# Kernel tuning notes

Measured on AMD Instinct MI355X. Metric: run time of the kernel, lower is better.

## Reference

```python
import jax, jax.numpy as jnp
import numpy as np

N_SPK, N_UTT, D = 512, 64, 1024
EPS = 1e-6  # matches tf.math.l2_normalize default epsilon guard


def _l2norm(x, axis=-1):
    return x / jnp.sqrt(jnp.maximum(jnp.sum(x * x, axis=axis, keepdims=True), EPS))


def setup_inputs() -> dict:
    key = jax.random.key(0)
    k1, _ = jax.random.split(key)
    inputs = jax.random.normal(k1, (N_SPK, N_UTT, D), dtype=jnp.float32)
    w = jnp.asarray(10.0, dtype=jnp.float32)
    b = jnp.asarray(-5.0, dtype=jnp.float32)
    return {"inputs": inputs, "w": w, "b": b}


def reference(inputs, w, b):
    N, M, _ = inputs.shape
    # speaker centroids: mean over utterances -> [N, D]
    centroids = jnp.mean(inputs, axis=1)
    # utterance (exclusion) centroids: mean of the other M-1 utterances -> [N, M, D]
    ut_centroids = (jnp.sum(inputs, axis=1, keepdims=True) - inputs) / (M - 1)

    e = _l2norm(inputs)          # [N, M, D]
    c = _l2norm(centroids)       # [N, D]
    uc = _l2norm(ut_centroids)   # [N, M, D]

    # cosine sim of every utterance vs every speaker centroid -> [N, M, K]
    cos_all = jnp.einsum('nmd,kd->nmk', e, c)
    # same-speaker entries use the self-exclusion centroid
    cos_self = jnp.sum(e * uc, axis=-1)  # [N, M]
    eye = jnp.eye(N, dtype=inputs.dtype)[:, None, :]  # [N, 1, N]
    cos_sim = cos_all * (1.0 - eye) + cos_self[:, :, None] * eye

    sim = w * cos_sim + b  # [N, M, N]
    # softmax contrastive loss: -S_{j,i,j} + logsumexp_k S_{j,i,k}, summed
    lse = jax.nn.logsumexp(sim, axis=-1)            # [N, M]
    pos = jnp.einsum('nmn->nm', sim)                # diagonal along speaker axes
    loss = jnp.sum(lse - pos)
    return loss
```

## Files before the change

### kernel.cpp

```cpp
#include <hip/hip_runtime.h>
#include <stdint.h>

#define N_SPK 512
#define N_UTT 64
#define DIM   1024
#define NROWS (N_SPK * N_UTT)
#define EPS   1e-6f

#define BM 128
#define BN 128
#define BK 32
#define KTILES (DIM / BK)

typedef __attribute__((ext_vector_type(8))) short short8;
typedef __attribute__((ext_vector_type(4))) float f32x4;

__device__ __forceinline__ uint16_t f2bf(float f) {
    union { float f; uint32_t i; } un; un.f = f;
    uint32_t x = un.i;
    return (uint16_t)((x + 0x7fffu + ((x >> 16) & 1u)) >> 16);
}

__global__ __launch_bounds__(256) void prep_stream(
    const float* __restrict__ x, uint16_t* __restrict__ xb,
    float* __restrict__ Sg4, float* __restrict__ xxg)
{
    const int b    = blockIdx.x;
    const int n    = b >> 2;
    const int g    = b & 3;
    const int tid  = threadIdx.x;
    const int lane = tid & 63;
    const int w    = tid >> 6;

    const float* xn  = x  + (size_t)n * N_UTT * DIM;
    uint16_t*    xbn = xb + (size_t)n * N_UTT * DIM;
    const int m0 = g * 16 + w * 4;

    float4 v[16];
    #pragma unroll
    for (int i = 0; i < 4; ++i)
        #pragma unroll
        for (int j = 0; j < 4; ++j)
            v[i * 4 + j] = *(const float4*)(xn + (size_t)(m0 + i) * DIM + j * 256 + lane * 4);

    float Sp[16];
    #pragma unroll
    for (int j = 0; j < 16; ++j) Sp[j] = 0.f;
    float xx[4] = {0.f, 0.f, 0.f, 0.f};

    #pragma unroll
    for (int i = 0; i < 4; ++i) {
        #pragma unroll
        for (int j = 0; j < 4; ++j) {
            const float4 q = v[i * 4 + j];
            xx[i] += q.x * q.x + q.y * q.y + q.z * q.z + q.w * q.w;
            Sp[j * 4 + 0] += q.x; Sp[j * 4 + 1] += q.y;
            Sp[j * 4 + 2] += q.z; Sp[j * 4 + 3] += q.w;
            ushort4 o;
            o.x = f2bf(q.x); o.y = f2bf(q.y); o.z = f2bf(q.z); o.w = f2bf(q.w);
            *(ushort4*)(xbn + (size_t)(m0 + i) * DIM + j * 256 + lane * 4) = o;
        }
    }

    #pragma unroll
    for (int i = 0; i < 4; ++i) {
        float t = xx[i];
        #pragma unroll
        for (int off = 1; off < 64; off <<= 1) t += __shfl_xor(t, off);
        if (lane == 0) xxg[n * N_UTT + m0 + i] = t;
    }

    __shared__ float Sh[4][DIM];
    #pragma unroll
    for (int j = 0; j < 4; ++j)
        *(float4*)&Sh[w][j * 256 + lane * 4] =
            make_float4(Sp[j * 4], Sp[j * 4 + 1], Sp[j * 4 + 2], Sp[j * 4 + 3]);
    __syncthreads();

    const int d0 = tid * 4;
    float4 a = *(const float4*)&Sh[0][d0];
    const float4 b1 = *(const float4*)&Sh[1][d0];
    const float4 b2 = *(const float4*)&Sh[2][d0];
    const float4 b3 = *(const float4*)&Sh[3][d0];
    a.x += b1.x + b2.x + b3.x; a.y += b1.y + b2.y + b3.y;
    a.z += b1.z + b2.z + b3.z; a.w += b1.w + b2.w + b3.w;
    *(float4*)(Sg4 + ((size_t)g * N_SPK + n) * DIM + d0) = a;
}

__global__ __launch_bounds__(256) void centroid_kernel(
    const float* __restrict__ Sg4, uint16_t* __restrict__ cmat, float* __restrict__ ssqg)
{
    const int n   = blockIdx.x;
    const int tid = threadIdx.x;
    const int d0  = tid * 4;

    float4 S = *(const float4*)(Sg4 + ((size_t)0 * N_SPK + n) * DIM + d0);
    #pragma unroll
    for (int g = 1; g < 4; ++g) {
        const float4 p = *(const float4*)(Sg4 + ((size_t)g * N_SPK + n) * DIM + d0);
        S.x += p.x; S.y += p.y; S.z += p.z; S.w += p.w;
    }

    float css = S.x * S.x + S.y * S.y + S.z * S.z + S.w * S.w;
    #pragma unroll
    for (int off = 1; off < 64; off <<= 1) css += __shfl_xor(css, off);
    __shared__ float red[4];
    if ((tid & 63) == 0) red[tid >> 6] = css;
    __syncthreads();
    const float ssq = red[0] + red[1] + red[2] + red[3];

    const float scale = rsqrtf(fmaxf(ssq * (1.0f / 4096.f), EPS)) * (1.0f / 64.f);
    ushort4 o;
    o.x = f2bf(S.x * scale); o.y = f2bf(S.y * scale);
    o.z = f2bf(S.z * scale); o.w = f2bf(S.w * scale);
    *(ushort4*)(cmat + (size_t)n * DIM + d0) = o;
    if (tid == 0) ssqg[n] = ssq;
}

__global__ __launch_bounds__(256) void gemm_lse_kernel(
    const uint16_t* __restrict__ xb, const uint16_t* __restrict__ cmat,
    const float* __restrict__ xxg, const float* __restrict__ ssqg,
    const float* __restrict__ wp, const float* __restrict__ bp,
    float* __restrict__ sumexp4, float* __restrict__ pos)
{
    __shared__ uint16_t Asm[BM * BK];
    __shared__ uint16_t Bsm[BN * BK];
    __shared__ float    SeLDS[BM];

    const int tid   = threadIdx.x;
    const int lane  = tid & 63;
    const int wid   = tid >> 6;
    const int waveM = wid >> 1;
    const int waveN = wid & 1;

    const int bid = blockIdx.x;
    const int rt  = (bid & 7) | ((bid >> 5) << 3);
    const int ct  = (bid >> 3) & 3;

    const int rowBase = rt * BM;
    const int colBase = ct * BN;

    const uint16_t* gA[2];
    const uint16_t* gB[2];
    #pragma unroll
    for (int i = 0; i < 2; ++i) {
        const int s    = i * 256 + tid;
        const int srow = s >> 2;
        const int kc   = (s & 3) ^ ((srow >> 1) & 3);
        gA[i] = xb   + (size_t)(rowBase + srow) * DIM + kc * 8;
        gB[i] = cmat + (size_t)(colBase + srow) * DIM + kc * 8;
    }

    f32x4 acc[4][4];
    #pragma unroll
    for (int i = 0; i < 4; ++i)
        #pragma unroll
        for (int j = 0; j < 4; ++j)
            acc[i][j] = (f32x4){0.f, 0.f, 0.f, 0.f};

    const int cL  = lane & 15;
    const int q   = lane >> 4;
    const int key = (cL >> 1) & 3;
    const int kcs = q ^ key;

    for (int kt = 0; kt < KTILES; ++kt) {
        __syncthreads();
        const int ko = kt * BK;
        #pragma unroll
        for (int i = 0; i < 2; ++i) {
            __builtin_amdgcn_global_load_lds(
                (const __attribute__((address_space(1))) void*)(gA[i] + ko),
                (__attribute__((address_space(3))) void*)(&Asm[(i * 256 + wid * 64) * 8]),
                16, 0, 0);
            __builtin_amdgcn_global_load_lds(
                (const __attribute__((address_space(1))) void*)(gB[i] + ko),
                (__attribute__((address_space(3))) void*)(&Bsm[(i * 256 + wid * 64) * 8]),
                16, 0, 0);
        }
        __syncthreads();

        short8 a[4], b[4];
        #pragma unroll
        for (int bi = 0; bi < 4; ++bi)
            a[bi] = *(const short8*)&Asm[(waveM * 64 + bi * 16 + cL) * BK + kcs * 8];
        #pragma unroll
        for (int bj = 0; bj < 4; ++bj)
            b[bj] = *(const short8*)&Bsm[(waveN * 64 + bj * 16 + cL) * BK + kcs * 8];

        #pragma unroll
        for (int bi = 0; bi < 4; ++bi)
            #pragma unroll
            for (int bj = 0; bj < 4; ++bj)
                acc[bi][bj] = __builtin_amdgcn_mfma_f32_16x16x32_bf16(
                    a[bi], b[bj], acc[bi][bj], 0, 0, 0);
    }

    const float wv = wp[0], bv = bp[0];
    float srow[16];
    #pragma unroll
    for (int bi = 0; bi < 4; ++bi) {
        #pragma unroll
        for (int r = 0; r < 4; ++r) {
            const int R     = rowBase + waveM * 64 + bi * 16 + q * 4 + r;
            const float xxv = xxg[R];
            const float rn  = rsqrtf(fmaxf(xxv, EPS));
            const int nrow  = R >> 6;
            float s = 0.f;
            #pragma unroll
            for (int bj = 0; bj < 4; ++bj) {
                const int col = colBase + waveN * 64 + bj * 16 + cL;
                const float dot = acc[bi][bj][r];
                float sim;
                if (col == nrow) {
                    const float ssqv = ssqg[nrow];
                    const float xs   = dot * sqrtf(ssqv);
                    const float d2   = ssqv - 2.f * xs + xxv;
                    const float cs   = ((xs - xxv) * (1.f / 63.f)) * rn *
                                       rsqrtf(fmaxf(d2 * (1.f / 3969.f), EPS));
                    sim = wv * cs + bv;
                    pos[R] = sim;
                } else {
                    sim = wv * (dot * rn) + bv;
                }
                s += __expf(sim);
            }
            #pragma unroll
            for (int off = 1; off < 16; off <<= 1) s += __shfl_xor(s, off);
            srow[bi * 4 + r] = s;
        }
    }

    if (waveN == 1 && cL == 0) {
        #pragma unroll
        for (int bi = 0; bi < 4; ++bi)
            #pragma unroll
            for (int r = 0; r < 4; ++r)
                SeLDS[waveM * 64 + bi * 16 + q * 4 + r] = srow[bi * 4 + r];
    }
    __syncthreads();
    if (waveN == 0 && cL == 0) {
        #pragma unroll
        for (int bi = 0; bi < 4; ++bi)
            #pragma unroll
            for (int r = 0; r < 4; ++r) {
                const int lr = waveM * 64 + bi * 16 + q * 4 + r;
                sumexp4[(size_t)ct * NROWS + rowBase + lr] = srow[bi * 4 + r] + SeLDS[lr];
            }
    }
}

__global__ __launch_bounds__(1024) void finalize_kernel(
    const float* __restrict__ pos, const float* __restrict__ se4,
    float* __restrict__ out)
{
    const int tid = threadIdx.x;
    float acc = 0.f;
    for (int r = tid; r < NROWS; r += 1024) {
        const float s = se4[r] + se4[NROWS + r] + se4[2 * NROWS + r] + se4[3 * NROWS + r];
        acc += __logf(s) - pos[r];
    }
    #pragma unroll
    for (int off = 1; off < 64; off <<= 1) acc += __shfl_xor(acc, off);
    __shared__ float red[16];
    if ((tid & 63) == 0) red[tid >> 6] = acc;
    __syncthreads();
    if (tid == 0) {
        float t = 0.f;
        #pragma unroll
        for (int i = 0; i < 16; ++i) t += red[i];
        out[0] = t;
    }
}

extern "C" void kernel_launch(void* const* d_in, const int* in_sizes, int n_in,
                              void* d_out, int out_size, void* d_ws, size_t ws_size,
                              hipStream_t stream)
{
    const float* x  = (const float*)d_in[0];
    const float* wp = (const float*)d_in[1];
    const float* bp = (const float*)d_in[2];
    float* out = (float*)d_out;

    char* ws = (char*)d_ws;
    size_t off = 0;
    uint16_t* xb      = (uint16_t*)(ws + off); off += (size_t)NROWS * DIM * 2;
    uint16_t* cmat    = (uint16_t*)(ws + off); off += (size_t)N_SPK * DIM * 2;
    float*    Sg4     = (float*)(ws + off);    off += (size_t)4 * N_SPK * DIM * 4;
    float*    xxg     = (float*)(ws + off);    off += (size_t)NROWS * 4;
    float*    pos     = (float*)(ws + off);    off += (size_t)NROWS * 4;
    float*    sumexp4 = (float*)(ws + off);    off += (size_t)4 * NROWS * 4;
    float*    ssqg    = (float*)(ws + off);    off += (size_t)N_SPK * 4;

    prep_stream<<<N_SPK * 4, 256, 0, stream>>>(x, xb, Sg4, xxg);
    centroid_kernel<<<N_SPK, 256, 0, stream>>>(Sg4, cmat, ssqg);
    gemm_lse_kernel<<<(NROWS / BM) * (N_SPK / BN), 256, 0, stream>>>(
        xb, cmat, xxg, ssqg, wp, bp, sumexp4, pos);
    finalize_kernel<<<1, 1024, 0, stream>>>(pos, sumexp4, out);
}
```

Measured before the change: 272.1 us.

## Fuse prep and centroid kernels; split final reduction across many blocks

Each speaker is now handled by one block that loops over all 64 utterances. It converts them to bf16, computes norms, and produces the normalized centroid directly. This removes the Sg4 partial-sum buffer and the separate centroid kernel launch. The single-block finalize is replaced by a 128-block partial reduction plus a tiny final sum, so the log/sum pass runs in parallel across the GPU. The trade-off is fewer blocks in the prep stage (512 instead of 2048), each with a serial loop, which reduces memory-level parallelism in a bandwidth-bound pass. The change also adds one extra small launch.

New measurement: 260.4 us. -4.3%, faster.

```diff
diff --git a/kernel.cpp b/kernel.cpp
--- a/kernel.cpp
+++ b/kernel.cpp
@@ -21,53 +21,56 @@
     return (uint16_t)((x + 0x7fffu + ((x >> 16) & 1u)) >> 16);
 }
 
-__global__ __launch_bounds__(256) void prep_stream(
+__global__ __launch_bounds__(256) void prep_centroid(
     const float* __restrict__ x, uint16_t* __restrict__ xb,
-    float* __restrict__ Sg4, float* __restrict__ xxg)
-{
-    const int b    = blockIdx.x;
-    const int n    = b >> 2;
-    const int g    = b & 3;
+    uint16_t* __restrict__ cmat, float* __restrict__ xxg,
+    float* __restrict__ ssqg)
+{
+    const int n    = blockIdx.x;
     const int tid  = threadIdx.x;
     const int lane = tid & 63;
     const int w    = tid >> 6;
 
     const float* xn  = x  + (size_t)n * N_UTT * DIM;
     uint16_t*    xbn = xb + (size_t)n * N_UTT * DIM;
-    const int m0 = g * 16 + w * 4;
-
-    float4 v[16];
-    #pragma unroll
-    for (int i = 0; i < 4; ++i)
-        #pragma unroll
-        for (int j = 0; j < 4; ++j)
-            v[i * 4 + j] = *(const float4*)(xn + (size_t)(m0 + i) * DIM + j * 256 + lane * 4);
 
     float Sp[16];
     #pragma unroll
     for (int j = 0; j < 16; ++j) Sp[j] = 0.f;
-    float xx[4] = {0.f, 0.f, 0.f, 0.f};
-
-    #pragma unroll
-    for (int i = 0; i < 4; ++i) {
-        #pragma unroll
-        for (int j = 0; j < 4; ++j) {
-            const float4 q = v[i * 4 + j];
-            xx[i] += q.x * q.x + q.y * q.y + q.z * q.z + q.w * q.w;
-            Sp[j * 4 + 0] += q.x; Sp[j * 4 + 1] += q.y;
-            Sp[j * 4 + 2] += q.z; Sp[j * 4 + 3] += q.w;
-            ushort4 o;
-            o.x = f2bf(q.x); o.y = f2bf(q.y); o.z = f2bf(q.z); o.w = f2bf(q.w);
-            *(ushort4*)(xbn + (size_t)(m0 + i) * DIM + j * 256 + lane * 4) = o;
-        }
-    }
-
-    #pragma unroll
-    for (int i = 0; i < 4; ++i) {
-        float t = xx[i];
-        #pragma unroll
-        for (int off = 1; off < 64; off <<= 1) t += __shfl_xor(t, off);
-        if (lane == 0) xxg[n * N_UTT + m0 + i] = t;
+
+    #pragma unroll 1
+    for (int o = 0; o < 4; ++o) {
+        const int m0 = w * 16 + o * 4;
+
+        float4 v[16];
+        #pragma unroll
+        for (int i = 0; i < 4; ++i)
+            #pragma unroll
+            for (int j = 0; j < 4; ++j)
+                v[i * 4 + j] = *(const float4*)(xn + (size_t)(m0 + i) * DIM + j * 256 + lane * 4);
+
+        float xx[4] = {0.f, 0.f, 0.f, 0.f};
+        #pragma unroll
+        for (int i = 0; i < 4; ++i) {
+            #pragma unroll
+            for (int j = 0; j < 4; ++j) {
+                const float4 q = v[i * 4 + j];
+                xx[i] += q.x * q.x + q.y * q.y + q.z * q.z + q.w * q.w;
+                Sp[j * 4 + 0] += q.x; Sp[j * 4 + 1] += q.y;
+                Sp[j * 4 + 2] += q.z; Sp[j * 4 + 3] += q.w;
+                ushort4 ov;
+                ov.x = f2bf(q.x); ov.y = f2bf(q.y); ov.z = f2bf(q.z); ov.w = f2bf(q.w);
+                *(ushort4*)(xbn + (size_t)(m0 + i) * DIM + j * 256 + lane * 4) = ov;
+            }
+        }
+
+        #pragma unroll
+        for (int i = 0; i < 4; ++i) {
+            float t = xx[i];
+            #pragma unroll
+            for (int off = 1; off < 64; off <<= 1) t += __shfl_xor(t, off);
+            if (lane == 0) xxg[n * N_UTT + m0 + i] = t;
+        }
     }
 
     __shared__ float Sh[4][DIM];
@@ -78,28 +81,12 @@
     __syncthreads();
 
     const int d0 = tid * 4;
-    float4 a = *(const float4*)&Sh[0][d0];
+    float4 S  = *(const float4*)&Sh[0][d0];
     const float4 b1 = *(const float4*)&Sh[1][d0];
     const float4 b2 = *(const float4*)&Sh[2][d0];
     const float4 b3 = *(const float4*)&Sh[3][d0];
-    a.x += b1.x + b2.x + b3.x; a.y += b1.y + b2.y + b3.y;
-    a.z += b1.z + b2.z + b3.z; a.w += b1.w + b2.w + b3.w;
-    *(float4*)(Sg4 + ((size_t)g * N_SPK + n) * DIM + d0) = a;
-}
-
-__global__ __launch_bounds__(256) void centroid_kernel(
-    const float* __restrict__ Sg4, uint16_t* __restrict__ cmat, float* __restrict__ ssqg)
-{
-    const int n   = blockIdx.x;
-    const int tid = threadIdx.x;
-    const int d0  = tid * 4;
-
-    float4 S = *(const float4*)(Sg4 + ((size_t)0 * N_SPK + n) * DIM + d0);
-    #pragma unroll
-    for (int g = 1; g < 4; ++g) {
-        const float4 p = *(const float4*)(Sg4 + ((size_t)g * N_SPK + n) * DIM + d0);
-        S.x += p.x; S.y += p.y; S.z += p.z; S.w += p.w;
-    }
+    S.x += b1.x + b2.x + b3.x; S.y += b1.y + b2.y + b3.y;
+    S.z += b1.z + b2.z + b3.z; S.w += b1.w + b2.w + b3.w;
 
     float css = S.x * S.x + S.y * S.y + S.z * S.z + S.w * S.w;
     #pragma unroll
@@ -110,10 +97,10 @@
     const float ssq = red[0] + red[1] + red[2] + red[3];
 
     const float scale = rsqrtf(fmaxf(ssq * (1.0f / 4096.f), EPS)) * (1.0f / 64.f);
-    ushort4 o;
-    o.x = f2bf(S.x * scale); o.y = f2bf(S.y * scale);
-    o.z = f2bf(S.z * scale); o.w = f2bf(S.w * scale);
-    *(ushort4*)(cmat + (size_t)n * DIM + d0) = o;
+    ushort4 oc;
+    oc.x = f2bf(S.x * scale); oc.y = f2bf(S.y * scale);
+    oc.z = f2bf(S.z * scale); oc.w = f2bf(S.w * scale);
+    *(ushort4*)(cmat + (size_t)n * DIM + d0) = oc;
     if (tid == 0) ssqg[n] = ssq;
 }
 
@@ -249,27 +236,33 @@
     }
 }
 
-__global__ __launch_bounds__(1024) void finalize_kernel(
+__global__ __launch_bounds__(256) void finalize_part(
     const float* __restrict__ pos, const float* __restrict__ se4,
-    float* __restrict__ out)
+    float* __restrict__ partial)
 {
     const int tid = threadIdx.x;
-    float acc = 0.f;
-    for (int r = tid; r < NROWS; r += 1024) {
-        const float s = se4[r] + se4[NROWS + r] + se4[2 * NROWS + r] + se4[3 * NROWS + r];
-        acc += __logf(s) - pos[r];
-    }
+    const int r   = blockIdx.x * 256 + tid;
+    const float s = se4[r] + se4[NROWS + r] + se4[2 * NROWS + r] + se4[3 * NROWS + r];
+    float acc = __logf(s) - pos[r];
     #pragma unroll
     for (int off = 1; off < 64; off <<= 1) acc += __shfl_xor(acc, off);
-    __shared__ float red[16];
+    __shared__ float red[4];
     if ((tid & 63) == 0) red[tid >> 6] = acc;
     __syncthreads();
-    if (tid == 0) {
-        float t = 0.f;
-        #pragma unroll
-        for (int i = 0; i < 16; ++i) t += red[i];
-        out[0] = t;
-    }
+    if (tid == 0) partial[blockIdx.x] = red[0] + red[1] + red[2] + red[3];
+}
+
+__global__ __launch_bounds__(128) void finalize_sum(
+    const float* __restrict__ partial, float* __restrict__ out)
+{
+    const int tid = threadIdx.x;
+    float t = partial[tid];
+    #pragma unroll
+    for (int off = 1; off < 64; off <<= 1) t += __shfl_xor(t, off);
+    __shared__ float red[2];
+    if ((tid & 63) == 0) red[tid >> 6] = t;
+    __syncthreads();
+    if (tid == 0) out[0] = red[0] + red[1];
 }
 
 extern "C" void kernel_launch(void* const* d_in, const int* in_sizes, int n_in,
@@ -285,15 +278,15 @@
     size_t off = 0;
     uint16_t* xb      = (uint16_t*)(ws + off); off += (size_t)NROWS * DIM * 2;
     uint16_t* cmat    = (uint16_t*)(ws + off); off += (size_t)N_SPK * DIM * 2;
-    float*    Sg4     = (float*)(ws + off);    off += (size_t)4 * N_SPK * DIM * 4;
     float*    xxg     = (float*)(ws + off);    off += (size_t)NROWS * 4;
     float*    pos     = (float*)(ws + off);    off += (size_t)NROWS * 4;
     float*    sumexp4 = (float*)(ws + off);    off += (size_t)4 * NROWS * 4;
     float*    ssqg    = (float*)(ws + off);    off += (size_t)N_SPK * 4;
-
-    prep_stream<<<N_SPK * 4, 256, 0, stream>>>(x, xb, Sg4, xxg);
-    centroid_kernel<<<N_SPK, 256, 0, stream>>>(Sg4, cmat, ssqg);
+    float*    partial = (float*)(ws + off);    off += (size_t)128 * 4;
+
+    prep_centroid<<<N_SPK, 256, 0, stream>>>(x, xb, cmat, xxg, ssqg);
     gemm_lse_kernel<<<(NROWS / BM) * (N_SPK / BN), 256, 0, stream>>>(
         xb, cmat, xxg, ssqg, wp, bp, sumexp4, pos);
-    finalize_kernel<<<1, 1024, 0, stream>>>(pos, sumexp4, out);
-}
+    finalize_part<<<NROWS / 256, 256, 0, stream>>>(pos, sumexp4, partial);
+    finalize_sum<<<1, 128, 0, stream>>>(partial, out);
+}
```
